# Kernel optimization log

Hardware: AMD Instinct MI355X
Metric: run time of the kernel (lower is better)

The kernel has to match this reference:

```python
import jax, jax.numpy as jnp
import numpy as np

B = 256   # number of segments
P = 2000  # points per segment (hard-coded by fc_1 = Linear(2000*32, 1024))
C = 32    # point feature channels
EPS_BN = 1e-5


def _bn_relu(h, g, b):
    # BatchNorm1d in training mode: batch statistics over axis 0, biased variance.
    m = jnp.mean(h, axis=0)
    v = jnp.var(h, axis=0)
    return jax.nn.relu((h - m) * jax.lax.rsqrt(v + EPS_BN) * g + b)


def setup_inputs() -> dict:
    key = jax.random.key(0)
    ks = jax.random.split(key, 16)
    s = 0.02
    inp = {
        "x": jax.random.normal(ks[0], (B * P, C), jnp.float32),
        "length": jnp.full((B,), P, dtype=jnp.int32),
        # attention MLP (1x1 conv1d chain 32->16->8->1), torch layout [out,in]
        "w1": jax.random.normal(ks[1], (16, 32), jnp.float32) * s,
        "b1": jnp.zeros((16,), jnp.float32),
        "g1": jnp.ones((16,), jnp.float32),
        "be1": jnp.zeros((16,), jnp.float32),
        "w2": jax.random.normal(ks[2], (8, 16), jnp.float32) * s,
        "b2": jnp.zeros((8,), jnp.float32),
        "g2": jnp.ones((8,), jnp.float32),
        "be2": jnp.zeros((8,), jnp.float32),
        "w3": jax.random.normal(ks[3], (1, 8), jnp.float32) * s,
        "b3": jnp.zeros((1,), jnp.float32),
        "g3": jnp.ones((1,), jnp.float32),
        "be3": jnp.zeros((1,), jnp.float32),
        # FC head
        "fw1": jax.random.normal(ks[4], (1024, P * C), jnp.float32) * s,
        "fb1": jnp.zeros((1024,), jnp.float32),
        "fg1": jnp.ones((1024,), jnp.float32),
        "fbe1": jnp.zeros((1024,), jnp.float32),
        "fw2": jax.random.normal(ks[5], (256, 1024), jnp.float32) * s,
        "fb2": jnp.zeros((256,), jnp.float32),
        "fg2": jnp.ones((256,), jnp.float32),
        "fbe2": jnp.zeros((256,), jnp.float32),
    }
    return inp


def reference(x, length, w1, b1, g1, be1, w2, b2, g2, be2, w3, b3, g3, be3,
              fw1, fb1, fg1, fbe1, fw2, fb2, fg2, fbe2):
    # Pointwise attention score MLP over all points (BN stats over the full
    # point dimension, matching conv1d+BatchNorm1d with batch size 1).
    h = _bn_relu(x @ w1.T + b1, g1, be1)          # [N,16]
    h = _bn_relu(h @ w2.T + b2, g2, be2)          # [N,8]
    score = _bn_relu(h @ w3.T + b3, g3, be3)      # [N,1]

    # Per-segment softmax over the point dim, then weighted features + flatten.
    # All segments have exactly P=2000 points (required by fc_1's input dim),
    # so the ragged slicing collapses to a dense [B,P,*] reshape.
    att = jax.nn.softmax(score.reshape(B, P, 1), axis=1)   # [B,P,1]
    pooled = (x.reshape(B, P, C) * att).reshape(B, P * C)  # [B,64000]

    r = _bn_relu(pooled @ fw1.T + fb1, fg1, fbe1)  # [B,1024]
    r = _bn_relu(r @ fw2.T + fb2, fg2, fbe2)       # [B,256]

    # F.normalize(p=2, dim=1, eps=1e-12)
    norm = jnp.maximum(jnp.linalg.norm(r, axis=1, keepdims=True), 1e-12)
    return r / norm
```

## Files before the change

kernel.cpp:

```cpp
#include <hip/hip_runtime.h>
#include <hip/hip_bf16.h>

#define NPTS   512000
#define PSEG   2000
#define INV_N  (1.0f/512000.0f)
#define EPS_BN 1e-5f

#define S1_OFF 0
#define S2_OFF 1024
#define S3_OFF 1536
#define S4_OFF 1600
#define S5_OFF 9792

using u32 = unsigned int;
using u16 = unsigned short;
using f32x4  = __attribute__((ext_vector_type(4))) float;
using bf16x8 = __attribute__((ext_vector_type(8))) short;

static __device__ __forceinline__ u16 f2bf(float f) {
    u32 u = __builtin_bit_cast(u32, f);
    u += 0x7fffu + ((u >> 16) & 1u);
    return (u16)(u >> 16);
}

static __device__ __forceinline__ void gload_lds16(const void* g, void* l) {
    __builtin_amdgcn_global_load_lds(
        (const __attribute__((address_space(1))) unsigned int*)g,
        (__attribute__((address_space(3))) unsigned int*)l, 16, 0, 0);
}

__global__ __launch_bounds__(256) void k_zero(float4* __restrict__ p) {
    p[blockIdx.x * 256 + threadIdx.x] = float4{0.0f, 0.0f, 0.0f, 0.0f};
}

__global__ __launch_bounds__(256) void k_mlp1(const float* __restrict__ x,
                                              const float* __restrict__ w1,
                                              float* __restrict__ a1,
                                              float* __restrict__ stats) {
    __shared__ float w[512];
    __shared__ float part[4][32];
    const int t = threadIdx.x;
    w[t] = w1[t]; w[t + 256] = w1[t + 256];
    __syncthreads();

    const int idx = blockIdx.x * 256 + t;
    const float4* xr = (const float4*)(x + (size_t)idx * 32);
    float4 xv[8];
#pragma unroll
    for (int i = 0; i < 8; i++) xv[i] = xr[i];

    float h[16];
#pragma unroll
    for (int c = 0; c < 16; c++) {
        float s = 0.0f;
        const float4* wr = (const float4*)(w + c * 32);
#pragma unroll
        for (int i = 0; i < 8; i++) {
            float4 wv = wr[i];
            s += xv[i].x * wv.x + xv[i].y * wv.y + xv[i].z * wv.z + xv[i].w * wv.w;
        }
        h[c] = s;
    }

    float4* ar = (float4*)(a1 + (size_t)idx * 16);
#pragma unroll
    for (int i = 0; i < 4; i++) {
        float4 o; o.x = h[i*4+0]; o.y = h[i*4+1]; o.z = h[i*4+2]; o.w = h[i*4+3];
        ar[i] = o;
    }

    const int lane = t & 63, wave = t >> 6;
#pragma unroll
    for (int c = 0; c < 16; c++) {
        float s = h[c], q = h[c] * h[c];
#pragma unroll
        for (int off = 32; off > 0; off >>= 1) {
            s += __shfl_down(s, off);
            q += __shfl_down(q, off);
        }
        if (lane == 0) { part[wave][c] = s; part[wave][16 + c] = q; }
    }
    __syncthreads();
    if (t < 32) {
        float tot = part[0][t] + part[1][t] + part[2][t] + part[3][t];
        atomicAdd(&stats[S1_OFF + (blockIdx.x & 31) * 32 + t], tot);
    }
}

__global__ __launch_bounds__(256) void k_mlp2(const float* __restrict__ a1,
                                              const float* __restrict__ w2,
                                              const float* __restrict__ g1,
                                              const float* __restrict__ be1,
                                              float* __restrict__ a2,
                                              float* __restrict__ stats) {
    __shared__ float w[128];
    __shared__ float sc[16], sh[16];
    __shared__ float part[4][16];
    const int t = threadIdx.x;
    if (t < 128) w[t] = w2[t];
    if (t < 16) {
        float s = 0.0f, q = 0.0f;
#pragma unroll 8
        for (int c = 0; c < 32; c++) {
            s += stats[S1_OFF + c * 32 + t];
            q += stats[S1_OFF + c * 32 + 16 + t];
        }
        float m = s * INV_N;
        float v = q * INV_N - m * m;
        float sl = g1[t] * rsqrtf(v + EPS_BN);
        sc[t] = sl; sh[t] = be1[t] - m * sl;
    }
    __syncthreads();

    const int idx = blockIdx.x * 256 + t;
    const float4* ar = (const float4*)(a1 + (size_t)idx * 16);
    float h[16];
#pragma unroll
    for (int i = 0; i < 4; i++) {
        float4 v4 = ar[i];
        h[i*4+0] = v4.x; h[i*4+1] = v4.y; h[i*4+2] = v4.z; h[i*4+3] = v4.w;
    }
#pragma unroll
    for (int c = 0; c < 16; c++) h[c] = fmaxf(fmaf(h[c], sc[c], sh[c]), 0.0f);

    float o[8];
#pragma unroll
    for (int c = 0; c < 8; c++) {
        float s = 0.0f;
#pragma unroll
        for (int k = 0; k < 16; k++) s += h[k] * w[c * 16 + k];
        o[c] = s;
    }
    float4* orp = (float4*)(a2 + (size_t)idx * 8);
    float4 o0; o0.x=o[0]; o0.y=o[1]; o0.z=o[2]; o0.w=o[3];
    float4 o1; o1.x=o[4]; o1.y=o[5]; o1.z=o[6]; o1.w=o[7];
    orp[0] = o0; orp[1] = o1;

    const int lane = t & 63, wave = t >> 6;
#pragma unroll
    for (int c = 0; c < 8; c++) {
        float s = o[c], q = o[c] * o[c];
#pragma unroll
        for (int off = 32; off > 0; off >>= 1) {
            s += __shfl_down(s, off);
            q += __shfl_down(q, off);
        }
        if (lane == 0) { part[wave][c] = s; part[wave][8 + c] = q; }
    }
    __syncthreads();
    if (t < 16) {
        float tot = part[0][t] + part[1][t] + part[2][t] + part[3][t];
        atomicAdd(&stats[S2_OFF + (blockIdx.x & 31) * 16 + t], tot);
    }
}

__global__ __launch_bounds__(256) void k_mlp3(const float* __restrict__ a2,
                                              const float* __restrict__ w3,
                                              const float* __restrict__ g2,
                                              const float* __restrict__ be2,
                                              float* __restrict__ a3,
                                              float* __restrict__ stats) {
    __shared__ float w[8], sc[8], sh[8];
    __shared__ float part[4][2];
    const int t = threadIdx.x;
    if (t < 8) {
        w[t] = w3[t];
        float s = 0.0f, q = 0.0f;
#pragma unroll 8
        for (int c = 0; c < 32; c++) {
            s += stats[S2_OFF + c * 16 + t];
            q += stats[S2_OFF + c * 16 + 8 + t];
        }
        float m = s * INV_N;
        float v = q * INV_N - m * m;
        float sl = g2[t] * rsqrtf(v + EPS_BN);
        sc[t] = sl; sh[t] = be2[t] - m * sl;
    }
    __syncthreads();

    const int idx = blockIdx.x * 256 + t;
    const float4* ar = (const float4*)(a2 + (size_t)idx * 8);
    float4 v0 = ar[0], v1 = ar[1];
    float h[8] = {v0.x, v0.y, v0.z, v0.w, v1.x, v1.y, v1.z, v1.w};
    float s = 0.0f;
#pragma unroll
    for (int c = 0; c < 8; c++) s += fmaxf(fmaf(h[c], sc[c], sh[c]), 0.0f) * w[c];
    a3[idx] = s;

    const int lane = t & 63, wave = t >> 6;
    float q = s * s;
    float ss = s;
#pragma unroll
    for (int off = 32; off > 0; off >>= 1) {
        ss += __shfl_down(ss, off);
        q  += __shfl_down(q, off);
    }
    if (lane == 0) { part[wave][0] = ss; part[wave][1] = q; }
    __syncthreads();
    if (t < 2) {
        float tot = part[0][t] + part[1][t] + part[2][t] + part[3][t];
        atomicAdd(&stats[S3_OFF + (blockIdx.x & 31) * 2 + t], tot);
    }
}

__global__ __launch_bounds__(256) void k_pool(const float* __restrict__ a3,
                                              const float* __restrict__ x,
                                              const float* __restrict__ g3,
                                              const float* __restrict__ be3,
                                              const float* __restrict__ stats,
                                              u16* __restrict__ pooled) {
    const int b = blockIdx.x, t = threadIdx.x;
    float sm = 0.0f, sq = 0.0f;
#pragma unroll 8
    for (int c = 0; c < 32; c++) {
        sm += stats[S3_OFF + c * 2];
        sq += stats[S3_OFF + c * 2 + 1];
    }
    const float m  = sm * INV_N;
    const float v  = sq * INV_N - m * m;
    const float sc = g3[0] * rsqrtf(v + EPS_BN);
    const float sh = be3[0] - m * sc;

    float sv[8];
    float mx = -1e30f;
#pragma unroll
    for (int i = 0; i < 8; i++) {
        int p = t + i * 256;
        if (p < PSEG) {
            float val = fmaxf(fmaf(a3[(size_t)b * PSEG + p], sc, sh), 0.0f);
            sv[i] = val; mx = fmaxf(mx, val);
        } else sv[i] = -1e30f;
    }
    const int lane = t & 63, wave = t >> 6;
    __shared__ float redm[4], reds[4];
#pragma unroll
    for (int off = 32; off > 0; off >>= 1) mx = fmaxf(mx, __shfl_xor(mx, off));
    if (lane == 0) redm[wave] = mx;
    __syncthreads();
    mx = fmaxf(fmaxf(redm[0], redm[1]), fmaxf(redm[2], redm[3]));

    float es = 0.0f;
#pragma unroll
    for (int i = 0; i < 8; i++) {
        int p = t + i * 256;
        if (p < PSEG) { float e = __expf(sv[i] - mx); sv[i] = e; es += e; }
    }
#pragma unroll
    for (int off = 32; off > 0; off >>= 1) es += __shfl_xor(es, off);
    if (lane == 0) reds[wave] = es;
    __syncthreads();
    const float inv = 1.0f / (reds[0] + reds[1] + reds[2] + reds[3]);

    const int swz = (b & 7) << 3;
#pragma unroll
    for (int i = 0; i < 8; i++) {
        int p = t + i * 256;
        if (p >= PSEG) continue;
        const float att = sv[i] * inv;
        const float4* xr = (const float4*)(x + ((size_t)b * PSEG + p) * 32);
        u16* dst = pooled + (size_t)b * 64000 + (size_t)(p >> 1) * 64;
        const int half = (p & 1) << 5;
#pragma unroll
        for (int u = 0; u < 4; u++) {
            float4 f0 = xr[u * 2], f1 = xr[u * 2 + 1];
            u32 q0 = (u32)f2bf(f0.x * att) | ((u32)f2bf(f0.y * att) << 16);
            u32 q1 = (u32)f2bf(f0.z * att) | ((u32)f2bf(f0.w * att) << 16);
            u32 q2 = (u32)f2bf(f1.x * att) | ((u32)f2bf(f1.y * att) << 16);
            u32 q3 = (u32)f2bf(f1.z * att) | ((u32)f2bf(f1.w * att) << 16);
            uint4 q; q.x = q0; q.y = q1; q.z = q2; q.w = q3;
            *(uint4*)(dst + ((half | (u << 3)) ^ swz)) = q;
        }
    }
}

__global__ __launch_bounds__(256) void k_gemm4(const u16* __restrict__ pooled,
                                               const float* __restrict__ fw1,
                                               float* __restrict__ a4p) {
    __shared__ alignas(16) char smem[49152];

    const int t = threadIdx.x;
    const int jblk = blockIdx.x;
    const int kblk = blockIdx.y;
    const int wave = t >> 6, lane = t & 63;
    const int kbase = kblk * 1600;

    const u16* gA = pooled + (size_t)(wave * 8 + (lane >> 3)) * 64000 + (lane & 7) * 8;
    const int jj = t >> 4;
    const int ks = (t & 15) * 4;
    const float* gB = fw1 + (size_t)(jblk * 64 + jj) * 64000 + ks;

    f32x4 acc[4][4] = {};
    float4 b0, b1, b2, b3;

#pragma unroll
    for (int i = 0; i < 8; i++)
        gload_lds16(gA + kbase + (size_t)i * 32 * 64000,
                    smem + wave * 1024 + i * 4096);
    {
        const float* bs = gB + kbase;
        b0 = *(const float4*)(bs);
        b1 = *(const float4*)(bs + (size_t)16 * 64000);
        b2 = *(const float4*)(bs + (size_t)32 * 64000);
        b3 = *(const float4*)(bs + (size_t)48 * 64000);
        char* Bs = smem + 32768;
#pragma unroll
        for (int i = 0; i < 4; i++) {
            const int j = i * 16 + jj;
            float4 v = (i == 0) ? b0 : (i == 1) ? b1 : (i == 2) ? b2 : b3;
            ushort4 bv;
            bv.x = f2bf(v.x); bv.y = f2bf(v.y); bv.z = f2bf(v.z); bv.w = f2bf(v.w);
            *(ushort4*)(Bs + ((j * 128 + ks * 2) ^ ((j & 7) << 4))) = bv;
        }
    }
    asm volatile("s_waitcnt vmcnt(0) lgkmcnt(0)" ::: "memory");
    __builtin_amdgcn_s_barrier();
    __builtin_amdgcn_sched_barrier(0);

    int cur = 0;
    for (int step = 0; step < 25; ++step) {
        const bool pf = (step + 1 < 25);
        if (pf) {
            const float* bs = gB + kbase + (step + 1) * 64;
            b0 = *(const float4*)(bs);
            b1 = *(const float4*)(bs + (size_t)16 * 64000);
            b2 = *(const float4*)(bs + (size_t)32 * 64000);
            b3 = *(const float4*)(bs + (size_t)48 * 64000);
        }
        __builtin_amdgcn_sched_barrier(0);
        const char* As = smem;
        const char* Bs = smem + 32768 + cur * 8192;
#pragma unroll
        for (int kk = 0; kk < 2; ++kk) {
            const int krow = kk * 32 + (lane >> 4) * 8;
            bf16x8 aF[4], bF[4];
#pragma unroll
            for (int mm = 0; mm < 4; mm++) {
                const int row = wave * 64 + mm * 16 + (lane & 15);
                aF[mm] = *(const bf16x8*)(As + ((row * 128 + krow * 2) ^ ((row & 7) << 4)));
            }
#pragma unroll
            for (int nn = 0; nn < 4; nn++) {
                const int col = nn * 16 + (lane & 15);
                bF[nn] = *(const bf16x8*)(Bs + ((col * 128 + krow * 2) ^ ((col & 7) << 4)));
            }
#pragma unroll
            for (int mm = 0; mm < 4; mm++)
#pragma unroll
                for (int nn = 0; nn < 4; nn++)
                    acc[mm][nn] = __builtin_amdgcn_mfma_f32_16x16x32_bf16(
                        aF[mm], bF[nn], acc[mm][nn], 0, 0, 0);
        }
        __builtin_amdgcn_sched_barrier(0);
        __builtin_amdgcn_s_barrier();
        __builtin_amdgcn_sched_barrier(0);
        if (pf) {
#pragma unroll
            for (int i = 0; i < 8; i++)
                gload_lds16(gA + kbase + (step + 1) * 64 + (size_t)i * 32 * 64000,
                            smem + wave * 1024 + i * 4096);
            __builtin_amdgcn_sched_barrier(0);
            char* Bn = smem + 32768 + (cur ^ 1) * 8192;
#pragma unroll
            for (int i = 0; i < 4; i++) {
                const int j = i * 16 + jj;
                float4 v = (i == 0) ? b0 : (i == 1) ? b1 : (i == 2) ? b2 : b3;
                ushort4 bv;
                bv.x = f2bf(v.x); bv.y = f2bf(v.y); bv.z = f2bf(v.z); bv.w = f2bf(v.w);
                *(ushort4*)(Bn + ((j * 128 + ks * 2) ^ ((j & 7) << 4))) = bv;
            }
            __builtin_amdgcn_sched_barrier(0);
            asm volatile("s_waitcnt vmcnt(0) lgkmcnt(0)" ::: "memory");
            __builtin_amdgcn_s_barrier();
            __builtin_amdgcn_sched_barrier(0);
        }
        cur ^= 1;
    }

    float* dst = a4p + (size_t)kblk * 262144;
#pragma unroll
    for (int mm = 0; mm < 4; mm++)
#pragma unroll
        for (int nn = 0; nn < 4; nn++)
#pragma unroll
            for (int r = 0; r < 4; r++) {
                const int row = wave * 64 + mm * 16 + (lane >> 4) * 4 + r;
                const int col = jblk * 64 + nn * 16 + (lane & 15);
                dst[(size_t)row * 1024 + col] = acc[mm][nn][r];
            }
}

__global__ __launch_bounds__(256) void k_red4(const float* __restrict__ a4p,
                                              float* __restrict__ a4,
                                              float* __restrict__ stats) {
    const int i = blockIdx.x, t = threadIdx.x;
    float4 s = {0.0f, 0.0f, 0.0f, 0.0f};
#pragma unroll 8
    for (int kb = 0; kb < 40; kb++) {
        float4 v = *(const float4*)(a4p + (size_t)kb * 262144 + (size_t)i * 1024 + t * 4);
        s.x += v.x; s.y += v.y; s.z += v.z; s.w += v.w;
    }
    *(float4*)(a4 + (size_t)i * 1024 + t * 4) = s;
    const int j = t * 4;
    float* s4 = stats + S4_OFF + (i & 3) * 2048;
    atomicAdd(&s4[j + 0], s.x);
    atomicAdd(&s4[j + 1], s.y);
    atomicAdd(&s4[j + 2], s.z);
    atomicAdd(&s4[j + 3], s.w);
    atomicAdd(&s4[1024 + j + 0], s.x * s.x);
    atomicAdd(&s4[1024 + j + 1], s.y * s.y);
    atomicAdd(&s4[1024 + j + 2], s.z * s.z);
    atomicAdd(&s4[1024 + j + 3], s.w * s.w);
}

__global__ __launch_bounds__(256) void k_fc2(const float* __restrict__ a4,
                                             const float* __restrict__ fg1,
                                             const float* __restrict__ fbe1,
                                             const float* __restrict__ fw2,
                                             float* __restrict__ stats,
                                             float* __restrict__ a5) {
    __shared__ alignas(16) float h[1024];
    const int i = blockIdx.x, t = threadIdx.x;
#pragma unroll
    for (int u = 0; u < 4; u++) {
        const int k = u * 256 + t;
        float s = 0.0f, q = 0.0f;
#pragma unroll
        for (int c = 0; c < 4; c++) {
            s += stats[S4_OFF + c * 2048 + k];
            q += stats[S4_OFF + c * 2048 + 1024 + k];
        }
        float m  = s * (1.0f / 256.0f);
        float v  = q * (1.0f / 256.0f) - m * m;
        float sc = fg1[k] * rsqrtf(v + EPS_BN);
        float sh = fbe1[k] - m * sc;
        h[k] = fmaxf(fmaf(a4[(size_t)i * 1024 + k], sc, sh), 0.0f);
    }
    __syncthreads();
    const float4* wr = (const float4*)(fw2 + (size_t)t * 1024);
    const float4* hr = (const float4*)h;
    float s = 0.0f;
#pragma unroll 4
    for (int u = 0; u < 256; u++) {
        float4 w = wr[u], hv = hr[u];
        s += w.x * hv.x + w.y * hv.y + w.z * hv.z + w.w * hv.w;
    }
    a5[(size_t)i * 256 + t] = s;
    float* s5 = stats + S5_OFF + (i & 15) * 512;
    atomicAdd(&s5[t], s);
    atomicAdd(&s5[256 + t], s * s);
}

__global__ __launch_bounds__(256) void k_norm(const float* __restrict__ a5,
                                              const float* __restrict__ fg2,
                                              const float* __restrict__ fbe2,
                                              const float* __restrict__ stats,
                                              float* __restrict__ out) {
    const int i = blockIdx.x, t = threadIdx.x;
    float s = 0.0f, q2 = 0.0f;
#pragma unroll
    for (int c = 0; c < 16; c++) {
        s  += stats[S5_OFF + c * 512 + t];
        q2 += stats[S5_OFF + c * 512 + 256 + t];
    }
    float m  = s * (1.0f / 256.0f);
    float v  = q2 * (1.0f / 256.0f) - m * m;
    float sc = fg2[t] * rsqrtf(v + EPS_BN);
    float sh = fbe2[t] - m * sc;
    float r = fmaxf(fmaf(a5[(size_t)i * 256 + t], sc, sh), 0.0f);

    float q = r * r;
    const int lane = t & 63, wave = t >> 6;
#pragma unroll
    for (int off = 32; off > 0; off >>= 1) q += __shfl_xor(q, off);
    __shared__ float red[4];
    if (lane == 0) red[wave] = q;
    __syncthreads();
    float tot = red[0] + red[1] + red[2] + red[3];
    float nrm = fmaxf(sqrtf(tot), 1e-12f);
    out[(size_t)i * 256 + t] = r / nrm;
}

extern "C" void kernel_launch(void* const* d_in, const int* in_sizes, int n_in,
                              void* d_out, int out_size, void* d_ws, size_t ws_size,
                              hipStream_t stream) {
    const float* x   = (const float*)d_in[0];
    const float* w1  = (const float*)d_in[2];
    const float* g1  = (const float*)d_in[4];
    const float* be1 = (const float*)d_in[5];
    const float* w2  = (const float*)d_in[6];
    const float* g2  = (const float*)d_in[8];
    const float* be2 = (const float*)d_in[9];
    const float* w3  = (const float*)d_in[10];
    const float* g3  = (const float*)d_in[12];
    const float* be3 = (const float*)d_in[13];
    const float* fw1 = (const float*)d_in[14];
    const float* fg1 = (const float*)d_in[16];
    const float* fbe1= (const float*)d_in[17];
    const float* fw2 = (const float*)d_in[18];
    const float* fg2 = (const float*)d_in[20];
    const float* fbe2= (const float*)d_in[21];
    float* out = (float*)d_out;

    char* ws = (char*)d_ws;
    float* stats = (float*)ws;
    float* a4 = (float*)(ws + 73728);
    float* a5 = (float*)(ws + 73728 + 1048576);
    float* a4p = (float*)(ws + 73728 + 1048576 + 262144);
    char*  big = ws + 73728 + 1048576 + 262144 + 41943040;
    float* a1 = (float*)big;
    u16*   pooled = (u16*)big;
    float* a2 = (float*)(big + 32768000);
    float* a3 = (float*)(big + 32768000 + 16384000);

    k_zero<<<18, 256, 0, stream>>>((float4*)ws);
    k_mlp1<<<2000, 256, 0, stream>>>(x, w1, a1, stats);
    k_mlp2<<<2000, 256, 0, stream>>>(a1, w2, g1, be1, a2, stats);
    k_mlp3<<<2000, 256, 0, stream>>>(a2, w3, g2, be2, a3, stats);
    k_pool<<<256, 256, 0, stream>>>(a3, x, g3, be3, stats, pooled);
    k_gemm4<<<dim3(16, 40), 256, 0, stream>>>(pooled, fw1, a4p);
    k_red4<<<256, 256, 0, stream>>>(a4p, a4, stats);
    k_fc2<<<256, 256, 0, stream>>>(a4, fg1, fbe1, fw2, stats, a5);
    k_norm<<<256, 256, 0, stream>>>(a5, fg2, fbe2, stats, out);
}
```

Before: 267.9 us.

## Fuse attention MLP stages and pooling into one persistent kernel with grid barriers

Replaces the three pointwise MLP kernels and the pooling kernel with a single persistent kernel of 500 blocks. Each block keeps the activations for 1024 points in registers across the BatchNorm stages and uses software grid barriers on atomic counters to wait for the global statistics. This removes the a1/a2 intermediate writes and reads and three kernel launches. In exchange it depends on all 500 blocks being co-resident, since the spin barrier otherwise deadlocks, and it raises register pressure per thread.

After: 403.6 us. +50.6%, slower.

```diff
diff --git a/kernel.cpp b/kernel.cpp
--- a/kernel.cpp
+++ b/kernel.cpp
@@ -5,12 +5,14 @@
 #define PSEG   2000
 #define INV_N  (1.0f/512000.0f)
 #define EPS_BN 1e-5f
+#define GRID1  500u
 
 #define S1_OFF 0
 #define S2_OFF 1024
 #define S3_OFF 1536
 #define S4_OFF 1600
 #define S5_OFF 9792
+#define CTR_OFF 18000
 
 using u32 = unsigned int;
 using u16 = unsigned short;
@@ -29,50 +31,68 @@
         (__attribute__((address_space(3))) unsigned int*)l, 16, 0, 0);
 }
 
+static __device__ __forceinline__ float ldg_dev(const float* p) {
+    return __hip_atomic_load(p, __ATOMIC_RELAXED, __HIP_MEMORY_SCOPE_AGENT);
+}
+static __device__ __forceinline__ void stg_dev(float* p, float v) {
+    __hip_atomic_store(p, v, __ATOMIC_RELAXED, __HIP_MEMORY_SCOPE_AGENT);
+}
+
+static __device__ __forceinline__ void gbar(u32* ctr, u32 target) {
+    __syncthreads();
+    if (threadIdx.x == 0) {
+        __hip_atomic_fetch_add(ctr, 1u, __ATOMIC_RELEASE, __HIP_MEMORY_SCOPE_AGENT);
+        while (__hip_atomic_load(ctr, __ATOMIC_RELAXED, __HIP_MEMORY_SCOPE_AGENT) < target)
+            __builtin_amdgcn_s_sleep(2);
+    }
+    __syncthreads();
+}
+
 __global__ __launch_bounds__(256) void k_zero(float4* __restrict__ p) {
     p[blockIdx.x * 256 + threadIdx.x] = float4{0.0f, 0.0f, 0.0f, 0.0f};
 }
 
-__global__ __launch_bounds__(256) void k_mlp1(const float* __restrict__ x,
-                                              const float* __restrict__ w1,
-                                              float* __restrict__ a1,
-                                              float* __restrict__ stats) {
-    __shared__ float w[512];
+__global__ __launch_bounds__(256, 2) void k_mega1(
+    const float* __restrict__ x,
+    const float* __restrict__ w1, const float* __restrict__ g1, const float* __restrict__ be1,
+    const float* __restrict__ w2, const float* __restrict__ g2, const float* __restrict__ be2,
+    const float* __restrict__ w3, const float* __restrict__ g3, const float* __restrict__ be3,
+    float* __restrict__ stats, float* __restrict__ a3, u16* __restrict__ pooled)
+{
+    __shared__ float wbuf[512];
+    __shared__ float scs[16], shs[16];
     __shared__ float part[4][32];
-    const int t = threadIdx.x;
-    w[t] = w1[t]; w[t + 256] = w1[t + 256];
-    __syncthreads();
-
-    const int idx = blockIdx.x * 256 + t;
-    const float4* xr = (const float4*)(x + (size_t)idx * 32);
-    float4 xv[8];
-#pragma unroll
-    for (int i = 0; i < 8; i++) xv[i] = xr[i];
-
-    float h[16];
+    __shared__ float redm[4], reds[4];
+    const int t = threadIdx.x, bid = blockIdx.x;
+    const int lane = t & 63, wave = t >> 6;
+    u32* ctr = (u32*)(stats + CTR_OFF);
+
+    wbuf[t] = w1[t]; wbuf[t + 256] = w1[t + 256];
+    __syncthreads();
+    float h[4][16];
+#pragma unroll
+    for (int pp = 0; pp < 4; pp++) {
+        const int pt = bid * 1024 + pp * 256 + t;
+        const float4* xr = (const float4*)(x + (size_t)pt * 32);
+        float4 xv[8];
+#pragma unroll
+        for (int i = 0; i < 8; i++) xv[i] = xr[i];
+#pragma unroll
+        for (int c = 0; c < 16; c++) {
+            const float4* wr = (const float4*)(wbuf + c * 32);
+            float s = 0.0f;
+#pragma unroll
+            for (int i = 0; i < 8; i++) {
+                float4 wv = wr[i];
+                s += xv[i].x * wv.x + xv[i].y * wv.y + xv[i].z * wv.z + xv[i].w * wv.w;
+            }
+            h[pp][c] = s;
+        }
+    }
 #pragma unroll
     for (int c = 0; c < 16; c++) {
-        float s = 0.0f;
-        const float4* wr = (const float4*)(w + c * 32);
-#pragma unroll
-        for (int i = 0; i < 8; i++) {
-            float4 wv = wr[i];
-            s += xv[i].x * wv.x + xv[i].y * wv.y + xv[i].z * wv.z + xv[i].w * wv.w;
-        }
-        h[c] = s;
-    }
-
-    float4* ar = (float4*)(a1 + (size_t)idx * 16);
-#pragma unroll
-    for (int i = 0; i < 4; i++) {
-        float4 o; o.x = h[i*4+0]; o.y = h[i*4+1]; o.z = h[i*4+2]; o.w = h[i*4+3];
-        ar[i] = o;
-    }
-
-    const int lane = t & 63, wave = t >> 6;
-#pragma unroll
-    for (int c = 0; c < 16; c++) {
-        float s = h[c], q = h[c] * h[c];
+        float s = h[0][c] + h[1][c] + h[2][c] + h[3][c];
+        float q = h[0][c]*h[0][c] + h[1][c]*h[1][c] + h[2][c]*h[2][c] + h[3][c]*h[3][c];
 #pragma unroll
         for (int off = 32; off > 0; off >>= 1) {
             s += __shfl_down(s, off);
@@ -83,63 +103,41 @@
     __syncthreads();
     if (t < 32) {
         float tot = part[0][t] + part[1][t] + part[2][t] + part[3][t];
-        atomicAdd(&stats[S1_OFF + (blockIdx.x & 31) * 32 + t], tot);
-    }
-}
-
-__global__ __launch_bounds__(256) void k_mlp2(const float* __restrict__ a1,
-                                              const float* __restrict__ w2,
-                                              const float* __restrict__ g1,
-                                              const float* __restrict__ be1,
-                                              float* __restrict__ a2,
-                                              float* __restrict__ stats) {
-    __shared__ float w[128];
-    __shared__ float sc[16], sh[16];
-    __shared__ float part[4][16];
-    const int t = threadIdx.x;
-    if (t < 128) w[t] = w2[t];
+        atomicAdd(&stats[S1_OFF + (bid & 31) * 32 + t], tot);
+    }
+    gbar(ctr + 0, GRID1);
+
     if (t < 16) {
         float s = 0.0f, q = 0.0f;
 #pragma unroll 8
         for (int c = 0; c < 32; c++) {
-            s += stats[S1_OFF + c * 32 + t];
-            q += stats[S1_OFF + c * 32 + 16 + t];
-        }
-        float m = s * INV_N;
-        float v = q * INV_N - m * m;
+            s += ldg_dev(&stats[S1_OFF + c * 32 + t]);
+            q += ldg_dev(&stats[S1_OFF + c * 32 + 16 + t]);
+        }
+        float m = s * INV_N, v = q * INV_N - m * m;
         float sl = g1[t] * rsqrtf(v + EPS_BN);
-        sc[t] = sl; sh[t] = be1[t] - m * sl;
-    }
-    __syncthreads();
-
-    const int idx = blockIdx.x * 256 + t;
-    const float4* ar = (const float4*)(a1 + (size_t)idx * 16);
-    float h[16];
-#pragma unroll
-    for (int i = 0; i < 4; i++) {
-        float4 v4 = ar[i];
-        h[i*4+0] = v4.x; h[i*4+1] = v4.y; h[i*4+2] = v4.z; h[i*4+3] = v4.w;
-    }
-#pragma unroll
-    for (int c = 0; c < 16; c++) h[c] = fmaxf(fmaf(h[c], sc[c], sh[c]), 0.0f);
-
-    float o[8];
+        scs[t] = sl; shs[t] = be1[t] - m * sl;
+    }
+    if (t < 128) wbuf[t] = w2[t];
+    __syncthreads();
+    float o[4][8];
+#pragma unroll
+    for (int pp = 0; pp < 4; pp++) {
+#pragma unroll
+        for (int c = 0; c < 16; c++)
+            h[pp][c] = fmaxf(fmaf(h[pp][c], scs[c], shs[c]), 0.0f);
+#pragma unroll
+        for (int c = 0; c < 8; c++) {
+            float s = 0.0f;
+#pragma unroll
+            for (int k = 0; k < 16; k++) s += h[pp][k] * wbuf[c * 16 + k];
+            o[pp][c] = s;
+        }
+    }
 #pragma unroll
     for (int c = 0; c < 8; c++) {
-        float s = 0.0f;
-#pragma unroll
-        for (int k = 0; k < 16; k++) s += h[k] * w[c * 16 + k];
-        o[c] = s;
-    }
-    float4* orp = (float4*)(a2 + (size_t)idx * 8);
-    float4 o0; o0.x=o[0]; o0.y=o[1]; o0.z=o[2]; o0.w=o[3];
-    float4 o1; o1.x=o[4]; o1.y=o[5]; o1.z=o[6]; o1.w=o[7];
-    orp[0] = o0; orp[1] = o1;
-
-    const int lane = t & 63, wave = t >> 6;
-#pragma unroll
-    for (int c = 0; c < 8; c++) {
-        float s = o[c], q = o[c] * o[c];
+        float s = o[0][c] + o[1][c] + o[2][c] + o[3][c];
+        float q = o[0][c]*o[0][c] + o[1][c]*o[1][c] + o[2][c]*o[2][c] + o[3][c]*o[3][c];
 #pragma unroll
         for (int off = 32; off > 0; off >>= 1) {
             s += __shfl_down(s, off);
@@ -150,76 +148,65 @@
     __syncthreads();
     if (t < 16) {
         float tot = part[0][t] + part[1][t] + part[2][t] + part[3][t];
-        atomicAdd(&stats[S2_OFF + (blockIdx.x & 31) * 16 + t], tot);
-    }
-}
-
-__global__ __launch_bounds__(256) void k_mlp3(const float* __restrict__ a2,
-                                              const float* __restrict__ w3,
-                                              const float* __restrict__ g2,
-                                              const float* __restrict__ be2,
-                                              float* __restrict__ a3,
-                                              float* __restrict__ stats) {
-    __shared__ float w[8], sc[8], sh[8];
-    __shared__ float part[4][2];
-    const int t = threadIdx.x;
+        atomicAdd(&stats[S2_OFF + (bid & 31) * 16 + t], tot);
+    }
+    gbar(ctr + 1, GRID1);
+
     if (t < 8) {
-        w[t] = w3[t];
         float s = 0.0f, q = 0.0f;
 #pragma unroll 8
         for (int c = 0; c < 32; c++) {
-            s += stats[S2_OFF + c * 16 + t];
-            q += stats[S2_OFF + c * 16 + 8 + t];
-        }
-        float m = s * INV_N;
-        float v = q * INV_N - m * m;
+            s += ldg_dev(&stats[S2_OFF + c * 16 + t]);
+            q += ldg_dev(&stats[S2_OFF + c * 16 + 8 + t]);
+        }
+        float m = s * INV_N, v = q * INV_N - m * m;
         float sl = g2[t] * rsqrtf(v + EPS_BN);
-        sc[t] = sl; sh[t] = be2[t] - m * sl;
-    }
-    __syncthreads();
-
-    const int idx = blockIdx.x * 256 + t;
-    const float4* ar = (const float4*)(a2 + (size_t)idx * 8);
-    float4 v0 = ar[0], v1 = ar[1];
-    float h[8] = {v0.x, v0.y, v0.z, v0.w, v1.x, v1.y, v1.z, v1.w};
-    float s = 0.0f;
-#pragma unroll
-    for (int c = 0; c < 8; c++) s += fmaxf(fmaf(h[c], sc[c], sh[c]), 0.0f) * w[c];
-    a3[idx] = s;
-
-    const int lane = t & 63, wave = t >> 6;
-    float q = s * s;
-    float ss = s;
-#pragma unroll
-    for (int off = 32; off > 0; off >>= 1) {
-        ss += __shfl_down(ss, off);
-        q  += __shfl_down(q, off);
-    }
-    if (lane == 0) { part[wave][0] = ss; part[wave][1] = q; }
+        scs[t] = sl; shs[t] = be2[t] - m * sl;
+        wbuf[t] = w3[t];
+    }
+    __syncthreads();
+    float sv4[4];
+#pragma unroll
+    for (int pp = 0; pp < 4; pp++) {
+        float s = 0.0f;
+#pragma unroll
+        for (int c = 0; c < 8; c++)
+            s += fmaxf(fmaf(o[pp][c], scs[c], shs[c]), 0.0f) * wbuf[c];
+        sv4[pp] = s;
+        stg_dev(&a3[bid * 1024 + pp * 256 + t], s);
+    }
+    {
+        float s = sv4[0] + sv4[1] + sv4[2] + sv4[3];
+        float q = sv4[0]*sv4[0] + sv4[1]*sv4[1] + sv4[2]*sv4[2] + sv4[3]*sv4[3];
+#pragma unroll
+        for (int off = 32; off > 0; off >>= 1) {
+            s += __shfl_down(s, off);
+            q += __shfl_down(q, off);
+        }
+        if (lane == 0) { part[wave][0] = s; part[wave][1] = q; }
+    }
     __syncthreads();
     if (t < 2) {
         float tot = part[0][t] + part[1][t] + part[2][t] + part[3][t];
-        atomicAdd(&stats[S3_OFF + (blockIdx.x & 31) * 2 + t], tot);
-    }
-}
-
-__global__ __launch_bounds__(256) void k_pool(const float* __restrict__ a3,
-                                              const float* __restrict__ x,
-                                              const float* __restrict__ g3,
-                                              const float* __restrict__ be3,
-                                              const float* __restrict__ stats,
-                                              u16* __restrict__ pooled) {
-    const int b = blockIdx.x, t = threadIdx.x;
-    float sm = 0.0f, sq = 0.0f;
+        atomicAdd(&stats[S3_OFF + (bid & 31) * 2 + t], tot);
+    }
+    gbar(ctr + 2, GRID1);
+    if (bid >= 256) return;
+
+    if (t == 0) {
+        float sm = 0.0f, sq = 0.0f;
 #pragma unroll 8
-    for (int c = 0; c < 32; c++) {
-        sm += stats[S3_OFF + c * 2];
-        sq += stats[S3_OFF + c * 2 + 1];
-    }
-    const float m  = sm * INV_N;
-    const float v  = sq * INV_N - m * m;
-    const float sc = g3[0] * rsqrtf(v + EPS_BN);
-    const float sh = be3[0] - m * sc;
+        for (int c = 0; c < 32; c++) {
+            sm += ldg_dev(&stats[S3_OFF + c * 2]);
+            sq += ldg_dev(&stats[S3_OFF + c * 2 + 1]);
+        }
+        float m = sm * INV_N, v = sq * INV_N - m * m;
+        float sl = g3[0] * rsqrtf(v + EPS_BN);
+        scs[0] = sl; shs[0] = be3[0] - m * sl;
+    }
+    __syncthreads();
+    const float sc3 = scs[0], sh3 = shs[0];
+    const int b = bid;
 
     float sv[8];
     float mx = -1e30f;
@@ -227,12 +214,10 @@
     for (int i = 0; i < 8; i++) {
         int p = t + i * 256;
         if (p < PSEG) {
-            float val = fmaxf(fmaf(a3[(size_t)b * PSEG + p], sc, sh), 0.0f);
+            float val = fmaxf(fmaf(ldg_dev(&a3[(size_t)b * PSEG + p]), sc3, sh3), 0.0f);
             sv[i] = val; mx = fmaxf(mx, val);
         } else sv[i] = -1e30f;
     }
-    const int lane = t & 63, wave = t >> 6;
-    __shared__ float redm[4], reds[4];
 #pragma unroll
     for (int off = 32; off > 0; off >>= 1) mx = fmaxf(mx, __shfl_xor(mx, off));
     if (lane == 0) redm[wave] = mx;
@@ -506,17 +491,12 @@
     float* a4 = (float*)(ws + 73728);
     float* a5 = (float*)(ws + 73728 + 1048576);
     float* a4p = (float*)(ws + 73728 + 1048576 + 262144);
-    char*  big = ws + 73728 + 1048576 + 262144 + 41943040;
-    float* a1 = (float*)big;
-    u16*   pooled = (u16*)big;
-    float* a2 = (float*)(big + 32768000);
-    float* a3 = (float*)(big + 32768000 + 16384000);
+    u16*   pooled = (u16*)(ws + 73728 + 1048576 + 262144 + 41943040);
+    float* a3 = (float*)(ws + 73728 + 1048576 + 262144 + 41943040 + 32768000);
 
     k_zero<<<18, 256, 0, stream>>>((float4*)ws);
-    k_mlp1<<<2000, 256, 0, stream>>>(x, w1, a1, stats);
-    k_mlp2<<<2000, 256, 0, stream>>>(a1, w2, g1, be1, a2, stats);
-    k_mlp3<<<2000, 256, 0, stream>>>(a2, w3, g2, be2, a3, stats);
-    k_pool<<<256, 256, 0, stream>>>(a3, x, g3, be3, stats, pooled);
+    k_mega1<<<GRID1, 256, 0, stream>>>(x, w1, g1, be1, w2, g2, be2,
+                                       w3, g3, be3, stats, a3, pooled);
     k_gemm4<<<dim3(16, 40), 256, 0, stream>>>(pooled, fw1, a4p);
     k_red4<<<256, 256, 0, stream>>>(a4p, a4, stats);
     k_fc2<<<256, 256, 0, stream>>>(a4, fg1, fbe1, fw2, stats, a5);
```

## Recompute attention MLP from x in each stats pass instead of storing intermediates

Applied to the files above, without the earlier changes.

Replaces the chain of MLP kernels that wrote a1/a2/a3 activations with three statistics-only passes and a pooling kernel that each recompute the pointwise MLP directly from x. Each pass accumulates only BN sums, removing the large intermediate writes and reads. The trade is reading x four times and recomputing earlier layers, with each stat kernel processing four points per thread over fewer blocks.

Result: slower. 602.0 us (+124.7%).

```diff
diff --git a/kernel.cpp b/kernel.cpp
--- a/kernel.cpp
+++ b/kernel.cpp
@@ -33,46 +33,40 @@
     p[blockIdx.x * 256 + threadIdx.x] = float4{0.0f, 0.0f, 0.0f, 0.0f};
 }
 
-__global__ __launch_bounds__(256) void k_mlp1(const float* __restrict__ x,
-                                              const float* __restrict__ w1,
-                                              float* __restrict__ a1,
-                                              float* __restrict__ stats) {
+
+__global__ __launch_bounds__(256) void k_stat1(const float* __restrict__ x,
+                                               const float* __restrict__ w1,
+                                               float* __restrict__ stats) {
     __shared__ float w[512];
     __shared__ float part[4][32];
-    const int t = threadIdx.x;
+    const int t = threadIdx.x, bid = blockIdx.x;
     w[t] = w1[t]; w[t + 256] = w1[t + 256];
     __syncthreads();
 
-    const int idx = blockIdx.x * 256 + t;
-    const float4* xr = (const float4*)(x + (size_t)idx * 32);
-    float4 xv[8];
-#pragma unroll
-    for (int i = 0; i < 8; i++) xv[i] = xr[i];
-
-    float h[16];
+    float sacc[16] = {}, qacc[16] = {};
+#pragma unroll
+    for (int pp = 0; pp < 4; pp++) {
+        const int pt = bid * 1024 + pp * 256 + t;
+        const float4* xr = (const float4*)(x + (size_t)pt * 32);
+        float4 xv[8];
+#pragma unroll
+        for (int i = 0; i < 8; i++) xv[i] = xr[i];
+#pragma unroll
+        for (int c = 0; c < 16; c++) {
+            const float4* wr = (const float4*)(w + c * 32);
+            float s = 0.0f;
+#pragma unroll
+            for (int i = 0; i < 8; i++) {
+                float4 wv = wr[i];
+                s += xv[i].x * wv.x + xv[i].y * wv.y + xv[i].z * wv.z + xv[i].w * wv.w;
+            }
+            sacc[c] += s; qacc[c] += s * s;
+        }
+    }
+    const int lane = t & 63, wave = t >> 6;
 #pragma unroll
     for (int c = 0; c < 16; c++) {
-        float s = 0.0f;
-        const float4* wr = (const float4*)(w + c * 32);
-#pragma unroll
-        for (int i = 0; i < 8; i++) {
-            float4 wv = wr[i];
-            s += xv[i].x * wv.x + xv[i].y * wv.y + xv[i].z * wv.z + xv[i].w * wv.w;
-        }
-        h[c] = s;
-    }
-
-    float4* ar = (float4*)(a1 + (size_t)idx * 16);
-#pragma unroll
-    for (int i = 0; i < 4; i++) {
-        float4 o; o.x = h[i*4+0]; o.y = h[i*4+1]; o.z = h[i*4+2]; o.w = h[i*4+3];
-        ar[i] = o;
-    }
-
-    const int lane = t & 63, wave = t >> 6;
-#pragma unroll
-    for (int c = 0; c < 16; c++) {
-        float s = h[c], q = h[c] * h[c];
+        float s = sacc[c], q = qacc[c];
 #pragma unroll
         for (int off = 32; off > 0; off >>= 1) {
             s += __shfl_down(s, off);
@@ -83,21 +77,23 @@
     __syncthreads();
     if (t < 32) {
         float tot = part[0][t] + part[1][t] + part[2][t] + part[3][t];
-        atomicAdd(&stats[S1_OFF + (blockIdx.x & 31) * 32 + t], tot);
-    }
-}
-
-__global__ __launch_bounds__(256) void k_mlp2(const float* __restrict__ a1,
-                                              const float* __restrict__ w2,
-                                              const float* __restrict__ g1,
-                                              const float* __restrict__ be1,
-                                              float* __restrict__ a2,
-                                              float* __restrict__ stats) {
-    __shared__ float w[128];
-    __shared__ float sc[16], sh[16];
+        atomicAdd(&stats[S1_OFF + (bid & 31) * 32 + t], tot);
+    }
+}
+
+__global__ __launch_bounds__(256) void k_stat2(const float* __restrict__ x,
+                                               const float* __restrict__ w1,
+                                               const float* __restrict__ w2,
+                                               const float* __restrict__ g1,
+                                               const float* __restrict__ be1,
+                                               float* __restrict__ stats) {
+    __shared__ float w[512];
+    __shared__ float wb[128];
+    __shared__ float sc1[16], sh1[16];
     __shared__ float part[4][16];
-    const int t = threadIdx.x;
-    if (t < 128) w[t] = w2[t];
+    const int t = threadIdx.x, bid = blockIdx.x;
+    w[t] = w1[t]; w[t + 256] = w1[t + 256];
+    if (t < 128) wb[t] = w2[t];
     if (t < 16) {
         float s = 0.0f, q = 0.0f;
 #pragma unroll 8
@@ -105,41 +101,44 @@
             s += stats[S1_OFF + c * 32 + t];
             q += stats[S1_OFF + c * 32 + 16 + t];
         }
-        float m = s * INV_N;
-        float v = q * INV_N - m * m;
+        float m = s * INV_N, v = q * INV_N - m * m;
         float sl = g1[t] * rsqrtf(v + EPS_BN);
-        sc[t] = sl; sh[t] = be1[t] - m * sl;
-    }
-    __syncthreads();
-
-    const int idx = blockIdx.x * 256 + t;
-    const float4* ar = (const float4*)(a1 + (size_t)idx * 16);
-    float h[16];
-#pragma unroll
-    for (int i = 0; i < 4; i++) {
-        float4 v4 = ar[i];
-        h[i*4+0] = v4.x; h[i*4+1] = v4.y; h[i*4+2] = v4.z; h[i*4+3] = v4.w;
-    }
-#pragma unroll
-    for (int c = 0; c < 16; c++) h[c] = fmaxf(fmaf(h[c], sc[c], sh[c]), 0.0f);
-
-    float o[8];
+        sc1[t] = sl; sh1[t] = be1[t] - m * sl;
+    }
+    __syncthreads();
+
+    float sacc[8] = {}, qacc[8] = {};
+#pragma unroll
+    for (int pp = 0; pp < 4; pp++) {
+        const int pt = bid * 1024 + pp * 256 + t;
+        const float4* xr = (const float4*)(x + (size_t)pt * 32);
+        float4 xv[8];
+#pragma unroll
+        for (int i = 0; i < 8; i++) xv[i] = xr[i];
+        float h[16];
+#pragma unroll
+        for (int c = 0; c < 16; c++) {
+            const float4* wr = (const float4*)(w + c * 32);
+            float s = 0.0f;
+#pragma unroll
+            for (int i = 0; i < 8; i++) {
+                float4 wv = wr[i];
+                s += xv[i].x * wv.x + xv[i].y * wv.y + xv[i].z * wv.z + xv[i].w * wv.w;
+            }
+            h[c] = fmaxf(fmaf(s, sc1[c], sh1[c]), 0.0f);
+        }
+#pragma unroll
+        for (int c = 0; c < 8; c++) {
+            float s = 0.0f;
+#pragma unroll
+            for (int k = 0; k < 16; k++) s += h[k] * wb[c * 16 + k];
+            sacc[c] += s; qacc[c] += s * s;
+        }
+    }
+    const int lane = t & 63, wave = t >> 6;
 #pragma unroll
     for (int c = 0; c < 8; c++) {
-        float s = 0.0f;
-#pragma unroll
-        for (int k = 0; k < 16; k++) s += h[k] * w[c * 16 + k];
-        o[c] = s;
-    }
-    float4* orp = (float4*)(a2 + (size_t)idx * 8);
-    float4 o0; o0.x=o[0]; o0.y=o[1]; o0.z=o[2]; o0.w=o[3];
-    float4 o1; o1.x=o[4]; o1.y=o[5]; o1.z=o[6]; o1.w=o[7];
-    orp[0] = o0; orp[1] = o1;
-
-    const int lane = t & 63, wave = t >> 6;
-#pragma unroll
-    for (int c = 0; c < 8; c++) {
-        float s = o[c], q = o[c] * o[c];
+        float s = sacc[c], q = qacc[c];
 #pragma unroll
         for (int off = 32; off > 0; off >>= 1) {
             s += __shfl_down(s, off);
@@ -150,76 +149,152 @@
     __syncthreads();
     if (t < 16) {
         float tot = part[0][t] + part[1][t] + part[2][t] + part[3][t];
-        atomicAdd(&stats[S2_OFF + (blockIdx.x & 31) * 16 + t], tot);
-    }
-}
-
-__global__ __launch_bounds__(256) void k_mlp3(const float* __restrict__ a2,
-                                              const float* __restrict__ w3,
-                                              const float* __restrict__ g2,
-                                              const float* __restrict__ be2,
-                                              float* __restrict__ a3,
-                                              float* __restrict__ stats) {
-    __shared__ float w[8], sc[8], sh[8];
+        atomicAdd(&stats[S2_OFF + (bid & 31) * 16 + t], tot);
+    }
+}
+
+__global__ __launch_bounds__(256) void k_stat3(const float* __restrict__ x,
+                                               const float* __restrict__ w1,
+                                               const float* __restrict__ w2,
+                                               const float* __restrict__ w3,
+                                               const float* __restrict__ g1,
+                                               const float* __restrict__ be1,
+                                               const float* __restrict__ g2,
+                                               const float* __restrict__ be2,
+                                               float* __restrict__ stats) {
+    __shared__ float w[512];
+    __shared__ float wb[128];
+    __shared__ float wc[8];
+    __shared__ float sc1[16], sh1[16], sc2[8], sh2[8];
     __shared__ float part[4][2];
-    const int t = threadIdx.x;
+    const int t = threadIdx.x, bid = blockIdx.x;
+    w[t] = w1[t]; w[t + 256] = w1[t + 256];
+    if (t < 128) wb[t] = w2[t];
+    if (t < 16) {
+        float s = 0.0f, q = 0.0f;
+#pragma unroll 8
+        for (int c = 0; c < 32; c++) {
+            s += stats[S1_OFF + c * 32 + t];
+            q += stats[S1_OFF + c * 32 + 16 + t];
+        }
+        float m = s * INV_N, v = q * INV_N - m * m;
+        float sl = g1[t] * rsqrtf(v + EPS_BN);
+        sc1[t] = sl; sh1[t] = be1[t] - m * sl;
+    }
     if (t < 8) {
-        w[t] = w3[t];
+        wc[t] = w3[t];
         float s = 0.0f, q = 0.0f;
 #pragma unroll 8
         for (int c = 0; c < 32; c++) {
             s += stats[S2_OFF + c * 16 + t];
             q += stats[S2_OFF + c * 16 + 8 + t];
         }
-        float m = s * INV_N;
-        float v = q * INV_N - m * m;
+        float m = s * INV_N, v = q * INV_N - m * m;
         float sl = g2[t] * rsqrtf(v + EPS_BN);
-        sc[t] = sl; sh[t] = be2[t] - m * sl;
-    }
-    __syncthreads();
-
-    const int idx = blockIdx.x * 256 + t;
-    const float4* ar = (const float4*)(a2 + (size_t)idx * 8);
-    float4 v0 = ar[0], v1 = ar[1];
-    float h[8] = {v0.x, v0.y, v0.z, v0.w, v1.x, v1.y, v1.z, v1.w};
-    float s = 0.0f;
-#pragma unroll
-    for (int c = 0; c < 8; c++) s += fmaxf(fmaf(h[c], sc[c], sh[c]), 0.0f) * w[c];
-    a3[idx] = s;
-
+        sc2[t] = sl; sh2[t] = be2[t] - m * sl;
+    }
+    __syncthreads();
+
+    float sacc = 0.0f, qacc = 0.0f;
+#pragma unroll
+    for (int pp = 0; pp < 4; pp++) {
+        const int pt = bid * 1024 + pp * 256 + t;
+        const float4* xr = (const float4*)(x + (size_t)pt * 32);
+        float4 xv[8];
+#pragma unroll
+        for (int i = 0; i < 8; i++) xv[i] = xr[i];
+        float h[16];
+#pragma unroll
+        for (int c = 0; c < 16; c++) {
+            const float4* wr = (const float4*)(w + c * 32);
+            float s = 0.0f;
+#pragma unroll
+            for (int i = 0; i < 8; i++) {
+                float4 wv = wr[i];
+                s += xv[i].x * wv.x + xv[i].y * wv.y + xv[i].z * wv.z + xv[i].w * wv.w;
+            }
+            h[c] = fmaxf(fmaf(s, sc1[c], sh1[c]), 0.0f);
+        }
+        float a3v = 0.0f;
+#pragma unroll
+        for (int c = 0; c < 8; c++) {
+            float s = 0.0f;
+#pragma unroll
+            for (int k = 0; k < 16; k++) s += h[k] * wb[c * 16 + k];
+            a3v += fmaxf(fmaf(s, sc2[c], sh2[c]), 0.0f) * wc[c];
+        }
+        sacc += a3v; qacc += a3v * a3v;
+    }
     const int lane = t & 63, wave = t >> 6;
-    float q = s * s;
-    float ss = s;
 #pragma unroll
     for (int off = 32; off > 0; off >>= 1) {
-        ss += __shfl_down(ss, off);
-        q  += __shfl_down(q, off);
-    }
-    if (lane == 0) { part[wave][0] = ss; part[wave][1] = q; }
+        sacc += __shfl_down(sacc, off);
+        qacc += __shfl_down(qacc, off);
+    }
+    if (lane == 0) { part[wave][0] = sacc; part[wave][1] = qacc; }
     __syncthreads();
     if (t < 2) {
         float tot = part[0][t] + part[1][t] + part[2][t] + part[3][t];
-        atomicAdd(&stats[S3_OFF + (blockIdx.x & 31) * 2 + t], tot);
-    }
-}
-
-__global__ __launch_bounds__(256) void k_pool(const float* __restrict__ a3,
-                                              const float* __restrict__ x,
+        atomicAdd(&stats[S3_OFF + (bid & 31) * 2 + t], tot);
+    }
+}
+
+__global__ __launch_bounds__(256) void k_pool(const float* __restrict__ x,
+                                              const float* __restrict__ w1,
+                                              const float* __restrict__ w2,
+                                              const float* __restrict__ w3,
+                                              const float* __restrict__ g1,
+                                              const float* __restrict__ be1,
+                                              const float* __restrict__ g2,
+                                              const float* __restrict__ be2,
                                               const float* __restrict__ g3,
                                               const float* __restrict__ be3,
                                               const float* __restrict__ stats,
                                               u16* __restrict__ pooled) {
+    __shared__ float w[512];
+    __shared__ float wb[128];
+    __shared__ float wc[8];
+    __shared__ float sc1[16], sh1[16], sc2[8], sh2[8], s3p[2];
+    __shared__ float redm[4], reds[4];
     const int b = blockIdx.x, t = threadIdx.x;
-    float sm = 0.0f, sq = 0.0f;
+    w[t] = w1[t]; w[t + 256] = w1[t + 256];
+    if (t < 128) wb[t] = w2[t];
+    if (t < 16) {
+        float s = 0.0f, q = 0.0f;
 #pragma unroll 8
-    for (int c = 0; c < 32; c++) {
-        sm += stats[S3_OFF + c * 2];
-        sq += stats[S3_OFF + c * 2 + 1];
-    }
-    const float m  = sm * INV_N;
-    const float v  = sq * INV_N - m * m;
-    const float sc = g3[0] * rsqrtf(v + EPS_BN);
-    const float sh = be3[0] - m * sc;
+        for (int c = 0; c < 32; c++) {
+            s += stats[S1_OFF + c * 32 + t];
+            q += stats[S1_OFF + c * 32 + 16 + t];
+        }
+        float m = s * INV_N, v = q * INV_N - m * m;
+        float sl = g1[t] * rsqrtf(v + EPS_BN);
+        sc1[t] = sl; sh1[t] = be1[t] - m * sl;
+    }
+    if (t < 8) {
+        wc[t] = w3[t];
+        float s = 0.0f, q = 0.0f;
+#pragma unroll 8
+        for (int c = 0; c < 32; c++) {
+            s += stats[S2_OFF + c * 16 + t];
+            q += stats[S2_OFF + c * 16 + 8 + t];
+        }
+        float m = s * INV_N, v = q * INV_N - m * m;
+        float sl = g2[t] * rsqrtf(v + EPS_BN);
+        sc2[t] = sl; sh2[t] = be2[t] - m * sl;
+    }
+    if (t == 0) {
+        float sm = 0.0f, sq = 0.0f;
+#pragma unroll 8
+        for (int c = 0; c < 32; c++) {
+            sm += stats[S3_OFF + c * 2];
+            sq += stats[S3_OFF + c * 2 + 1];
+        }
+        float m = sm * INV_N, v = sq * INV_N - m * m;
+        float sl = g3[0] * rsqrtf(v + EPS_BN);
+        s3p[0] = sl; s3p[1] = be3[0] - m * sl;
+    }
+    __syncthreads();
+    const float sc3 = s3p[0], sh3 = s3p[1];
 
     float sv[8];
     float mx = -1e30f;
@@ -227,12 +302,35 @@
     for (int i = 0; i < 8; i++) {
         int p = t + i * 256;
         if (p < PSEG) {
-            float val = fmaxf(fmaf(a3[(size_t)b * PSEG + p], sc, sh), 0.0f);
+            const float4* xr = (const float4*)(x + ((size_t)b * PSEG + p) * 32);
+            float4 xv[8];
+#pragma unroll
+            for (int u = 0; u < 8; u++) xv[u] = xr[u];
+            float h[16];
+#pragma unroll
+            for (int c = 0; c < 16; c++) {
+                const float4* wr = (const float4*)(w + c * 32);
+                float s = 0.0f;
+#pragma unroll
+                for (int u = 0; u < 8; u++) {
+                    float4 wv = wr[u];
+                    s += xv[u].x * wv.x + xv[u].y * wv.y + xv[u].z * wv.z + xv[u].w * wv.w;
+                }
+                h[c] = fmaxf(fmaf(s, sc1[c], sh1[c]), 0.0f);
+            }
+            float a3v = 0.0f;
+#pragma unroll
+            for (int c = 0; c < 8; c++) {
+                float s = 0.0f;
+#pragma unroll
+                for (int k = 0; k < 16; k++) s += h[k] * wb[c * 16 + k];
+                a3v += fmaxf(fmaf(s, sc2[c], sh2[c]), 0.0f) * wc[c];
+            }
+            float val = fmaxf(fmaf(a3v, sc3, sh3), 0.0f);
             sv[i] = val; mx = fmaxf(mx, val);
         } else sv[i] = -1e30f;
     }
     const int lane = t & 63, wave = t >> 6;
-    __shared__ float redm[4], reds[4];
 #pragma unroll
     for (int off = 32; off > 0; off >>= 1) mx = fmaxf(mx, __shfl_xor(mx, off));
     if (lane == 0) redm[wave] = mx;
@@ -506,17 +604,14 @@
     float* a4 = (float*)(ws + 73728);
     float* a5 = (float*)(ws + 73728 + 1048576);
     float* a4p = (float*)(ws + 73728 + 1048576 + 262144);
-    char*  big = ws + 73728 + 1048576 + 262144 + 41943040;
-    float* a1 = (float*)big;
-    u16*   pooled = (u16*)big;
-    float* a2 = (float*)(big + 32768000);
-    float* a3 = (float*)(big + 32768000 + 16384000);
+    u16*   pooled = (u16*)(ws + 73728 + 1048576 + 262144 + 41943040);
 
     k_zero<<<18, 256, 0, stream>>>((float4*)ws);
-    k_mlp1<<<2000, 256, 0, stream>>>(x, w1, a1, stats);
-    k_mlp2<<<2000, 256, 0, stream>>>(a1, w2, g1, be1, a2, stats);
-    k_mlp3<<<2000, 256, 0, stream>>>(a2, w3, g2, be2, a3, stats);
-    k_pool<<<256, 256, 0, stream>>>(a3, x, g3, be3, stats, pooled);
+    k_stat1<<<500, 256, 0, stream>>>(x, w1, stats);
+    k_stat2<<<500, 256, 0, stream>>>(x, w1, w2, g1, be1, stats);
+    k_stat3<<<500, 256, 0, stream>>>(x, w1, w2, w3, g1, be1, g2, be2, stats);
+    k_pool<<<256, 256, 0, stream>>>(x, w1, w2, w3, g1, be1, g2, be2, g3, be3,
+                                    stats, pooled);
     k_gemm4<<<dim3(16, 40), 256, 0, stream>>>(pooled, fw1, a4p);
     k_red4<<<256, 256, 0, stream>>>(a4p, a4, stats);
     k_fc2<<<256, 256, 0, stream>>>(a4, fg1, fbe1, fw2, stats, a5);
```
